# Performance work log

Measured on AMD Instinct MI355X. Metric: run time of the kernel, lower is better.

## Reference

```python
import jax, jax.numpy as jnp
import numpy as np

PIXEL_SIZE = 0.2        # Angstroms
WAVELENGTH = 0.025      # Angstroms
SLICE_THICKNESS = 2.0   # Angstroms
PH, PW = 128, 128       # probe shape


def _make_propagator(h, w, pixel, wl, dz):
    ky = jnp.fft.fftfreq(h, d=pixel).astype(jnp.float32)
    kx = jnp.fft.fftfreq(w, d=pixel).astype(jnp.float32)
    k2 = ky[:, None] ** 2 + kx[None, :] ** 2
    phase = (-jnp.pi * wl * dz) * k2
    return jnp.exp(1j * phase.astype(jnp.float32)).astype(jnp.complex64)


def setup_inputs() -> dict:
    key = jax.random.key(0)
    k0, k1, k2, k3, k4 = jax.random.split(key, 5)
    probe_real = jax.random.normal(k0, (4, PH, PW), jnp.float32)
    probe_imag = jax.random.normal(k1, (4, PH, PW), jnp.float32)
    obj_real = jax.random.normal(k2, (8, 512, 512), jnp.float32)
    obj_imag = jax.random.normal(k3, (8, 512, 512), jnp.float32)
    positions = jax.random.randint(k4, (512, 2), 0, 384).astype(jnp.int32)
    return {"probe_real": probe_real, "probe_imag": probe_imag,
            "obj_real": obj_real, "obj_imag": obj_imag,
            "positions": positions}


def reference(probe_real, probe_imag, obj_real, obj_imag, positions):
    probe = (probe_real + 1j * probe_imag).astype(jnp.complex64)  # (M,H,W)
    obj = (obj_real + 1j * obj_imag).astype(jnp.complex64)        # (S,Ho,Wo)
    num_slices = obj.shape[0]
    prop = _make_propagator(PH, PW, PIXEL_SIZE, WAVELENGTH, SLICE_THICKNESS)

    # Batched patch gather: (N, S, PH, PW)
    def get_patch(pos):
        return jax.lax.dynamic_slice(obj, (0, pos[0], pos[1]),
                                     (num_slices, PH, PW))
    patches = jax.vmap(get_patch)(positions)

    # Multislice: multiply slice 0, then [propagate, multiply] per slice.
    ex = probe[None, :, :, :] * patches[:, 0][:, None]  # (N,M,H,W)
    for s in range(1, num_slices):
        ex = jnp.fft.ifft2(jnp.fft.fft2(ex) * prop)
        ex = ex * patches[:, s][:, None]

    ex = jnp.fft.fftshift(jnp.fft.fft2(ex), axes=(-2, -1))
    intensities = jnp.sum(jnp.abs(ex) ** 2, axis=1)  # (N,H,W)
    return intensities.astype(jnp.float32)
```

## Files before the change

kernel.cpp:

```cpp
#include <hip/hip_runtime.h>
#include <hip/hip_fp16.h>
#include <math.h>

#define NT      1024
#define NPIX    16384
#define NSLICES 8
#define NMODES  4
#define OBJW    512
#define LSTR    136

typedef float v2f __attribute__((ext_vector_type(2)));

__device__ __forceinline__ v2f pk_add(v2f a, v2f b) {
    v2f d; asm("v_pk_add_f32 %0, %1, %2" : "=v"(d) : "v"(a), "v"(b)); return d;
}
__device__ __forceinline__ v2f pk_sub(v2f a, v2f b) {
    v2f d; asm("v_pk_add_f32 %0, %1, %2 neg_lo:[0,1] neg_hi:[0,1]"
               : "=v"(d) : "v"(a), "v"(b)); return d;
}
__device__ __forceinline__ v2f pk_fma(v2f a, v2f b, v2f c) {
    v2f d; asm("v_pk_fma_f32 %0, %1, %2, %3" : "=v"(d) : "v"(a), "v"(b), "v"(c)); return d;
}
__device__ __forceinline__ v2f pk_cmul(v2f a, v2f b) {
    v2f t, d;
    asm("v_pk_mul_f32 %0, %1, %2 op_sel:[0,0] op_sel_hi:[1,0]"
        : "=v"(t) : "v"(a), "v"(b));
    asm("v_pk_fma_f32 %0, %1, %2, %3 op_sel:[1,1,0] op_sel_hi:[0,1,1] neg_lo:[1,0,0]"
        : "=v"(d) : "v"(a), "v"(b), "v"(t));
    return d;
}
__device__ __forceinline__ v2f pk_cmulc(v2f a, v2f b) {
    v2f t, d;
    asm("v_pk_mul_f32 %0, %1, %2 op_sel:[0,0] op_sel_hi:[1,0]"
        : "=v"(t) : "v"(a), "v"(b));
    asm("v_pk_fma_f32 %0, %1, %2, %3 op_sel:[1,1,0] op_sel_hi:[0,1,1] neg_hi:[1,0,0]"
        : "=v"(d) : "v"(a), "v"(b), "v"(t));
    return d;
}
__device__ __forceinline__ v2f pk_mnegi(v2f a) { return (v2f){a.y, -a.x}; }
__device__ __forceinline__ v2f pk_mposi(v2f a) { return (v2f){-a.y, a.x}; }

__host__ __device__ constexpr int BR4(int p) {
    return ((p & 1) << 3) | ((p & 2) << 1) | ((p & 4) >> 1) | ((p & 8) >> 3);
}
__host__ __device__ constexpr int BR3(int c) {
    return ((c & 1) << 2) | (c & 2) | ((c & 4) >> 2);
}

__device__ __forceinline__ float xor1f(float x) {
    int i = __float_as_int(x);
    return __int_as_float(__builtin_amdgcn_update_dpp(i, i, 0xB1, 0xF, 0xF, false));
}
__device__ __forceinline__ float xor2f(float x) {
    int i = __float_as_int(x);
    return __int_as_float(__builtin_amdgcn_update_dpp(i, i, 0x4E, 0xF, 0xF, false));
}
__device__ __forceinline__ float xor4f(float x) {
    return __int_as_float(__builtin_amdgcn_ds_swizzle(__float_as_int(x), 0x101F));
}

__device__ __constant__ float FA_RE[8] = {1,1,1,1, 1.0f,  0.707106781f,  0.0f, -0.707106781f};
__device__ __constant__ float FA_IM[8] = {0,0,0,0, 0.0f, -0.707106781f, -1.0f, -0.707106781f};

__device__ __forceinline__ void fft16_fwd(v2f v[16], const v2f* W) {
    #pragma unroll
    for (int s = 8; s >= 1; s >>= 1) {
        #pragma unroll
        for (int q = 0; q < 16; q += 2 * s) {
            #pragma unroll
            for (int j = 0; j < s; j++) {
                const int tw = j * (8 / s);
                v2f u = v[q + j], w = v[q + j + s];
                v[q + j] = pk_add(u, w);
                v2f d = pk_sub(u, w);
                v[q + j + s] = (tw == 0) ? d
                             : (tw == 4) ? pk_mnegi(d)
                                         : pk_cmulc(d, W[tw]);
            }
        }
    }
}
__device__ __forceinline__ void fft16_inv(v2f v[16], const v2f* W) {
    #pragma unroll
    for (int s = 1; s <= 8; s <<= 1) {
        #pragma unroll
        for (int q = 0; q < 16; q += 2 * s) {
            #pragma unroll
            for (int j = 0; j < s; j++) {
                const int tw = j * (8 / s);
                v2f u = v[q + j], w = v[q + j + s];
                v2f tv = (tw == 0) ? w
                       : (tw == 4) ? pk_mposi(w)
                                   : pk_cmul(w, W[tw]);
                v[q + j]     = pk_add(u, tv);
                v[q + j + s] = pk_sub(u, tv);
            }
        }
    }
}

__device__ __forceinline__ void cross8_fwd(v2f v[16], v2f sAp, v2f sBp, v2f sCp,
                                           v2f fA, v2f rrf) {
    #pragma unroll
    for (int p = 0; p < 16; p++) {
        v2f o;
        o.x = xor4f(v[p].x); o.y = xor4f(v[p].y);
        v2f a = pk_fma(sAp, v[p], o);
        v2f b = pk_cmul(a, fA);
        o.x = xor2f(b.x); o.y = xor2f(b.y);
        v2f n = pk_fma(sBp, b, o);
        v2f r = pk_cmul(n, rrf);
        o.x = xor1f(r.x); o.y = xor1f(r.y);
        v[p] = pk_fma(sCp, r, o);
    }
}
__device__ __forceinline__ void cross8_inv(v2f v[16], v2f sAp, v2f sBp, v2f sCp,
                                           v2f fA, v2f rrf) {
    #pragma unroll
    for (int p = 0; p < 16; p++) {
        v2f o;
        o.x = xor1f(v[p].x); o.y = xor1f(v[p].y);
        v2f n = pk_fma(sCp, v[p], o);
        v2f r = pk_cmulc(n, rrf);
        o.x = xor2f(r.x); o.y = xor2f(r.y);
        v2f b = pk_fma(sBp, r, o);
        v2f a = pk_cmulc(b, fA);
        o.x = xor4f(a.x); o.y = xor4f(a.y);
        v[p] = pk_fma(sAp, a, o);
    }
}

__device__ __forceinline__ void pass_A_fwd(v2f v[16], int c, v2f sAp, v2f sBp,
                                           v2f sCp, v2f fA, v2f rrf,
                                           const v2f* W, const v2f* tA) {
    fft16_fwd(v, W);
    #pragma unroll
    for (int p = 0; p < 16; p++) v[p] = pk_cmul(v[p], tA[8 * p + c]);
    cross8_fwd(v, sAp, sBp, sCp, fA, rrf);
}
__device__ __forceinline__ void pass_A_inv(v2f v[16], int c, v2f sAp, v2f sBp,
                                           v2f sCp, v2f fA, v2f rrf,
                                           const v2f* W, const v2f* tA) {
    cross8_inv(v, sAp, sBp, sCp, fA, rrf);
    #pragma unroll
    for (int p = 0; p < 16; p++) v[p] = pk_cmulc(v[p], tA[8 * p + c]);
    fft16_inv(v, W);
}

__device__ __forceinline__ void pass_B_fwd(v2f v[16], int c, v2f sAp, v2f sBp,
                                           v2f sCp, v2f fA, v2f rrf,
                                           const v2f* W, const v2f* tB) {
    cross8_fwd(v, sAp, sBp, sCp, fA, rrf);
    #pragma unroll
    for (int i = 0; i < 16; i++) v[i] = pk_cmul(v[i], tB[8 * i + c]);
    fft16_fwd(v, W);
}
__device__ __forceinline__ void pass_B_inv(v2f v[16], int c, v2f sAp, v2f sBp,
                                           v2f sCp, v2f fA, v2f rrf,
                                           const v2f* W, const v2f* tB) {
    fft16_inv(v, W);
    #pragma unroll
    for (int i = 0; i < 16; i++) v[i] = pk_cmulc(v[i], tB[8 * i + c]);
    cross8_inv(v, sAp, sBp, sCp, fA, rrf);
}

__device__ __forceinline__ __half2 toh2(v2f a) {
    return __float22half2_rn(make_float2(a.x, a.y));
}
__device__ __forceinline__ v2f frh2(__half2 h) {
    float2 f = __half22float2(h);
    return (v2f){f.x, f.y};
}

__global__ void
__attribute__((amdgpu_flat_work_group_size(1024, 1024)))
multislice_kernel(const float* __restrict__ probe_re,
                  const float* __restrict__ probe_im,
                  const float* __restrict__ obj_re,
                  const float* __restrict__ obj_im,
                  const int*   __restrict__ positions,
                  float*       __restrict__ out)
{
    __shared__ __half2 LTH[128 * LSTR];
    __shared__ v2f     tA[128];
    __shared__ v2f     tB[128];
    __shared__ v2f     pytp[128];

    const int t  = threadIdx.x;
    const int g  = t >> 3;
    const int c  = t & 7;
    const int rc = BR3(c);
    const int gh = g >> 4;
    const int rho_g = ((g & 15) << 3) | gh;
    const int n  = blockIdx.x;
    const int Y0 = positions[2 * n];
    const int X0 = positions[2 * n + 1];

    if (t < 128) {
        int p_ = t >> 3, c_ = t & 7;
        float angA = -2.0f * 3.14159265358979323846f
                     * (float)(c_ * BR4(p_)) / 128.0f;
        float s, cc; __sincosf(angA, &s, &cc);
        tA[t] = (v2f){cc, s};
        float angB = -2.0f * 3.14159265358979323846f
                     * (float)(p_ * BR3(c_)) / 128.0f;
        __sincosf(angB, &s, &cc);
        tB[t] = (v2f){cc, s};
        int kh = BR3(c_) + 8 * BR4(p_);
        float fy = (float)(kh < 64 ? kh : kh - 128) * (1.0f / 25.6f);
        float ph = -0.15707963267948966f * fy * fy;
        float ps, pcs; __sincosf(ph, &ps, &pcs);
        pytp[t] = (v2f){pcs * (1.0f / 16384.0f), ps * (1.0f / 16384.0f)};
    }

    const float sA = (c < 4) ? 1.0f : -1.0f;
    const float sB = (c & 2) ? -1.0f : 1.0f;
    const float sC = (c & 1) ? -1.0f : 1.0f;
    const v2f sAp = {sA, sA}, sBp = {sB, sB}, sCp = {sC, sC};
    const v2f fA  = {FA_RE[c], FA_IM[c]};
    const v2f rrf = ((c & 3) == 3) ? (v2f){0.0f, -1.0f} : (v2f){1.0f, 0.0f};

    const v2f W[8] = {
        { 1.0f,         0.0f        },
        { 0.923879533f, 0.382683432f},
        { 0.707106781f, 0.707106781f},
        { 0.382683432f, 0.923879533f},
        { 0.0f,         1.0f        },
        {-0.382683432f, 0.923879533f},
        {-0.707106781f, 0.707106781f},
        {-0.923879533f, 0.382683432f},
    };

    float fx = (float)(g < 64 ? g : g - 128) * (1.0f / 25.6f);
    float phx = -0.15707963267948966f * fx * fx;
    float pxs, pxc; __sincosf(phx, &pxs, &pxc);
    const v2f px = {pxc, pxs};
    __syncthreads();

    const long long base = (long long)n * NPIX;
    const int a1w = rho_g ^ rc;
    const int a1r = g * LSTR + (c ^ gh);
    const int a2w = rho_g ^ c;
    const int a2r = g * LSTR + (rc ^ gh);

    v2f v[16];

    for (int m = 0; m < NMODES; m++) {
        __syncthreads();
        #pragma unroll
        for (int i = 0; i < 16; i++) {
            int w  = c + 8 * i;
            int pi = m * NPIX + g * 128 + w;
            v2f pr = {probe_re[pi], probe_im[pi]};
            int oi = (Y0 + g) * OBJW + X0 + w;
            v2f ob = {obj_re[oi], obj_im[oi]};
            v[i] = pk_cmul(pr, ob);
        }

        for (int s = 1; s < NSLICES; s++) {
            pass_A_fwd(v, c, sAp, sBp, sCp, fA, rrf, W, tA);
            #pragma unroll
            for (int p = 0; p < 16; p++) {
                int kw = BR4(p) + 16 * rc;
                LTH[kw * LSTR + a1w] = toh2(v[p]);
            }
            __syncthreads();
            #pragma unroll
            for (int i = 0; i < 16; i++)
                v[i] = frh2(LTH[a1r + 8 * i]);
            __syncthreads();
            pass_B_fwd(v, c, sAp, sBp, sCp, fA, rrf, W, tB);
            #pragma unroll
            for (int p = 0; p < 16; p++) {
                v2f pp = pk_cmul(pytp[8 * p + c], px);
                v[p] = pk_cmul(v[p], pp);
            }
            pass_B_inv(v, c, sAp, sBp, sCp, fA, rrf, W, tB);
            #pragma unroll
            for (int i = 0; i < 16; i++)
                LTH[(i + 16 * c) * LSTR + a2w] = toh2(v[i]);
            __syncthreads();
            #pragma unroll
            for (int p = 0; p < 16; p++)
                v[p] = frh2(LTH[a2r + 8 * BR4(p)]);
            __syncthreads();
            pass_A_inv(v, c, sAp, sBp, sCp, fA, rrf, W, tA);
            #pragma unroll
            for (int i = 0; i < 16; i++) {
                int w  = c + 8 * i;
                int oi = (s * OBJW + Y0 + g) * OBJW + X0 + w;
                v2f ob = {obj_re[oi], obj_im[oi]};
                v[i] = pk_cmul(v[i], ob);
            }
        }

        pass_A_fwd(v, c, sAp, sBp, sCp, fA, rrf, W, tA);
        #pragma unroll
        for (int p = 0; p < 16; p++) {
            int kw = BR4(p) + 16 * rc;
            LTH[kw * LSTR + a1w] = toh2(v[p]);
        }
        __syncthreads();
        #pragma unroll
        for (int i = 0; i < 16; i++)
            v[i] = frh2(LTH[a1r + 8 * i]);
        pass_B_fwd(v, c, sAp, sBp, sCp, fA, rrf, W, tB);
        #pragma unroll
        for (int p = 0; p < 16; p++) {
            int kh = BR3(c) + 8 * BR4(p);
            long long oidx = base + (long long)(((kh ^ 64) << 7) + (g ^ 64));
            float val = fmaf(v[p].x, v[p].x, v[p].y * v[p].y);
            if (m > 0) val += out[oidx];
            out[oidx] = val;
        }
    }
}

extern "C" void kernel_launch(void* const* d_in, const int* in_sizes, int n_in,
                              void* d_out, int out_size, void* d_ws, size_t ws_size,
                              hipStream_t stream) {
    const float* probe_re = (const float*)d_in[0];
    const float* probe_im = (const float*)d_in[1];
    const float* obj_re   = (const float*)d_in[2];
    const float* obj_im   = (const float*)d_in[3];
    const int*   pos      = (const int*)d_in[4];
    float* out = (float*)d_out;

    const int N = out_size / NPIX;
    multislice_kernel<<<dim3(N), dim3(NT), 0, stream>>>(
        probe_re, probe_im, obj_re, obj_im, pos, out);
}
```

Baseline: 1.225 ms.

## Process two probe modes per iteration with doubled LDS transpose buffers

Each thread now carries two probe modes (v and u) through the multislice FFT pipeline at once. Sharing twiddle loads, object loads and the barrier count between both modes halves the number of syncs and mode-loop iterations, and gives more independent instructions for latency hiding. The LDS transpose buffer is doubled and waves_per_eu(2) is requested to allow higher register use. The risk is register pressure and spills from holding 32 complex values per thread, plus more shared memory per block.

```diff
diff --git a/kernel.cpp b/kernel.cpp
--- a/kernel.cpp
+++ b/kernel.cpp
@@ -8,6 +8,7 @@
 #define NMODES  4
 #define OBJW    512
 #define LSTR    136
+#define BUF1    (128 * LSTR)
 
 typedef float v2f __attribute__((ext_vector_type(2)));
 
@@ -99,69 +100,106 @@
     }
 }
 
-__device__ __forceinline__ void cross8_fwd(v2f v[16], v2f sAp, v2f sBp, v2f sCp,
-                                           v2f fA, v2f rrf) {
+__device__ __forceinline__ void cross8_fwd2(v2f v[16], v2f u[16],
+                                            v2f sAp, v2f sBp, v2f sCp,
+                                            v2f fA, v2f rrf) {
     #pragma unroll
     for (int p = 0; p < 16; p++) {
-        v2f o;
+        v2f o, q;
         o.x = xor4f(v[p].x); o.y = xor4f(v[p].y);
-        v2f a = pk_fma(sAp, v[p], o);
-        v2f b = pk_cmul(a, fA);
-        o.x = xor2f(b.x); o.y = xor2f(b.y);
-        v2f n = pk_fma(sBp, b, o);
-        v2f r = pk_cmul(n, rrf);
-        o.x = xor1f(r.x); o.y = xor1f(r.y);
-        v[p] = pk_fma(sCp, r, o);
-    }
-}
-__device__ __forceinline__ void cross8_inv(v2f v[16], v2f sAp, v2f sBp, v2f sCp,
-                                           v2f fA, v2f rrf) {
+        q.x = xor4f(u[p].x); q.y = xor4f(u[p].y);
+        v2f a  = pk_fma(sAp, v[p], o);
+        v2f a2 = pk_fma(sAp, u[p], q);
+        v2f b  = pk_cmul(a,  fA);
+        v2f b2 = pk_cmul(a2, fA);
+        o.x = xor2f(b.x);  o.y = xor2f(b.y);
+        q.x = xor2f(b2.x); q.y = xor2f(b2.y);
+        v2f n  = pk_fma(sBp, b,  o);
+        v2f n2 = pk_fma(sBp, b2, q);
+        v2f r  = pk_cmul(n,  rrf);
+        v2f r2 = pk_cmul(n2, rrf);
+        o.x = xor1f(r.x);  o.y = xor1f(r.y);
+        q.x = xor1f(r2.x); q.y = xor1f(r2.y);
+        v[p] = pk_fma(sCp, r,  o);
+        u[p] = pk_fma(sCp, r2, q);
+    }
+}
+__device__ __forceinline__ void cross8_inv2(v2f v[16], v2f u[16],
+                                            v2f sAp, v2f sBp, v2f sCp,
+                                            v2f fA, v2f rrf) {
     #pragma unroll
     for (int p = 0; p < 16; p++) {
-        v2f o;
+        v2f o, q;
         o.x = xor1f(v[p].x); o.y = xor1f(v[p].y);
-        v2f n = pk_fma(sCp, v[p], o);
-        v2f r = pk_cmulc(n, rrf);
-        o.x = xor2f(r.x); o.y = xor2f(r.y);
-        v2f b = pk_fma(sBp, r, o);
-        v2f a = pk_cmulc(b, fA);
-        o.x = xor4f(a.x); o.y = xor4f(a.y);
-        v[p] = pk_fma(sAp, a, o);
-    }
-}
-
-__device__ __forceinline__ void pass_A_fwd(v2f v[16], int c, v2f sAp, v2f sBp,
-                                           v2f sCp, v2f fA, v2f rrf,
-                                           const v2f* W, const v2f* tA) {
-    fft16_fwd(v, W);
-    #pragma unroll
-    for (int p = 0; p < 16; p++) v[p] = pk_cmul(v[p], tA[8 * p + c]);
-    cross8_fwd(v, sAp, sBp, sCp, fA, rrf);
-}
-__device__ __forceinline__ void pass_A_inv(v2f v[16], int c, v2f sAp, v2f sBp,
-                                           v2f sCp, v2f fA, v2f rrf,
-                                           const v2f* W, const v2f* tA) {
-    cross8_inv(v, sAp, sBp, sCp, fA, rrf);
-    #pragma unroll
-    for (int p = 0; p < 16; p++) v[p] = pk_cmulc(v[p], tA[8 * p + c]);
-    fft16_inv(v, W);
-}
-
-__device__ __forceinline__ void pass_B_fwd(v2f v[16], int c, v2f sAp, v2f sBp,
-                                           v2f sCp, v2f fA, v2f rrf,
-                                           const v2f* W, const v2f* tB) {
-    cross8_fwd(v, sAp, sBp, sCp, fA, rrf);
-    #pragma unroll
-    for (int i = 0; i < 16; i++) v[i] = pk_cmul(v[i], tB[8 * i + c]);
-    fft16_fwd(v, W);
-}
-__device__ __forceinline__ void pass_B_inv(v2f v[16], int c, v2f sAp, v2f sBp,
-                                           v2f sCp, v2f fA, v2f rrf,
-                                           const v2f* W, const v2f* tB) {
-    fft16_inv(v, W);
-    #pragma unroll
-    for (int i = 0; i < 16; i++) v[i] = pk_cmulc(v[i], tB[8 * i + c]);
-    cross8_inv(v, sAp, sBp, sCp, fA, rrf);
+        q.x = xor1f(u[p].x); q.y = xor1f(u[p].y);
+        v2f n  = pk_fma(sCp, v[p], o);
+        v2f n2 = pk_fma(sCp, u[p], q);
+        v2f r  = pk_cmulc(n,  rrf);
+        v2f r2 = pk_cmulc(n2, rrf);
+        o.x = xor2f(r.x);  o.y = xor2f(r.y);
+        q.x = xor2f(r2.x); q.y = xor2f(r2.y);
+        v2f b  = pk_fma(sBp, r,  o);
+        v2f b2 = pk_fma(sBp, r2, q);
+        v2f a  = pk_cmulc(b,  fA);
+        v2f a2 = pk_cmulc(b2, fA);
+        o.x = xor4f(a.x);  o.y = xor4f(a.y);
+        q.x = xor4f(a2.x); q.y = xor4f(a2.y);
+        v[p] = pk_fma(sAp, a,  o);
+        u[p] = pk_fma(sAp, a2, q);
+    }
+}
+
+__device__ __forceinline__ void pass_A_fwd2(v2f v[16], v2f u[16], int c,
+                                            v2f sAp, v2f sBp, v2f sCp,
+                                            v2f fA, v2f rrf,
+                                            const v2f* W, const v2f* tA) {
+    fft16_fwd(v, W); fft16_fwd(u, W);
+    #pragma unroll
+    for (int p = 0; p < 16; p++) {
+        v2f w = tA[8 * p + c];
+        v[p] = pk_cmul(v[p], w);
+        u[p] = pk_cmul(u[p], w);
+    }
+    cross8_fwd2(v, u, sAp, sBp, sCp, fA, rrf);
+}
+__device__ __forceinline__ void pass_A_inv2(v2f v[16], v2f u[16], int c,
+                                            v2f sAp, v2f sBp, v2f sCp,
+                                            v2f fA, v2f rrf,
+                                            const v2f* W, const v2f* tA) {
+    cross8_inv2(v, u, sAp, sBp, sCp, fA, rrf);
+    #pragma unroll
+    for (int p = 0; p < 16; p++) {
+        v2f w = tA[8 * p + c];
+        v[p] = pk_cmulc(v[p], w);
+        u[p] = pk_cmulc(u[p], w);
+    }
+    fft16_inv(v, W); fft16_inv(u, W);
+}
+__device__ __forceinline__ void pass_B_fwd2(v2f v[16], v2f u[16], int c,
+                                            v2f sAp, v2f sBp, v2f sCp,
+                                            v2f fA, v2f rrf,
+                                            const v2f* W, const v2f* tB) {
+    cross8_fwd2(v, u, sAp, sBp, sCp, fA, rrf);
+    #pragma unroll
+    for (int i = 0; i < 16; i++) {
+        v2f w = tB[8 * i + c];
+        v[i] = pk_cmul(v[i], w);
+        u[i] = pk_cmul(u[i], w);
+    }
+    fft16_fwd(v, W); fft16_fwd(u, W);
+}
+__device__ __forceinline__ void pass_B_inv2(v2f v[16], v2f u[16], int c,
+                                            v2f sAp, v2f sBp, v2f sCp,
+                                            v2f fA, v2f rrf,
+                                            const v2f* W, const v2f* tB) {
+    fft16_inv(v, W); fft16_inv(u, W);
+    #pragma unroll
+    for (int i = 0; i < 16; i++) {
+        v2f w = tB[8 * i + c];
+        v[i] = pk_cmulc(v[i], w);
+        u[i] = pk_cmulc(u[i], w);
+    }
+    cross8_inv2(v, u, sAp, sBp, sCp, fA, rrf);
 }
 
 __device__ __forceinline__ __half2 toh2(v2f a) {
@@ -173,7 +211,7 @@
 }
 
 __global__ void
-__attribute__((amdgpu_flat_work_group_size(1024, 1024)))
+__attribute__((amdgpu_flat_work_group_size(1024, 1024), amdgpu_waves_per_eu(2)))
 multislice_kernel(const float* __restrict__ probe_re,
                   const float* __restrict__ probe_im,
                   const float* __restrict__ obj_re,
@@ -181,7 +219,7 @@
                   const int*   __restrict__ positions,
                   float*       __restrict__ out)
 {
-    __shared__ __half2 LTH[128 * LSTR];
+    __shared__ __half2 LTH[2 * 128 * LSTR];
     __shared__ v2f     tA[128];
     __shared__ v2f     tB[128];
     __shared__ v2f     pytp[128];
@@ -243,73 +281,89 @@
     const int a2w = rho_g ^ c;
     const int a2r = g * LSTR + (rc ^ gh);
 
-    v2f v[16];
-
-    for (int m = 0; m < NMODES; m++) {
-        __syncthreads();
+    v2f v[16], u[16];
+
+    for (int m = 0; m < NMODES; m += 2) {
         #pragma unroll
         for (int i = 0; i < 16; i++) {
             int w  = c + 8 * i;
-            int pi = m * NPIX + g * 128 + w;
-            v2f pr = {probe_re[pi], probe_im[pi]};
             int oi = (Y0 + g) * OBJW + X0 + w;
             v2f ob = {obj_re[oi], obj_im[oi]};
-            v[i] = pk_cmul(pr, ob);
+            int pi0 = m * NPIX + g * 128 + w;
+            v2f pr0 = {probe_re[pi0], probe_im[pi0]};
+            v[i] = pk_cmul(pr0, ob);
+            int pi1 = (m + 1) * NPIX + g * 128 + w;
+            v2f pr1 = {probe_re[pi1], probe_im[pi1]};
+            u[i] = pk_cmul(pr1, ob);
         }
 
         for (int s = 1; s < NSLICES; s++) {
-            pass_A_fwd(v, c, sAp, sBp, sCp, fA, rrf, W, tA);
+            pass_A_fwd2(v, u, c, sAp, sBp, sCp, fA, rrf, W, tA);
+            __syncthreads();
             #pragma unroll
             for (int p = 0; p < 16; p++) {
                 int kw = BR4(p) + 16 * rc;
-                LTH[kw * LSTR + a1w] = toh2(v[p]);
+                LTH[kw * LSTR + a1w]        = toh2(v[p]);
+                LTH[BUF1 + kw * LSTR + a1w] = toh2(u[p]);
             }
             __syncthreads();
             #pragma unroll
-            for (int i = 0; i < 16; i++)
+            for (int i = 0; i < 16; i++) {
                 v[i] = frh2(LTH[a1r + 8 * i]);
-            __syncthreads();
-            pass_B_fwd(v, c, sAp, sBp, sCp, fA, rrf, W, tB);
+                u[i] = frh2(LTH[BUF1 + a1r + 8 * i]);
+            }
+            pass_B_fwd2(v, u, c, sAp, sBp, sCp, fA, rrf, W, tB);
             #pragma unroll
             for (int p = 0; p < 16; p++) {
                 v2f pp = pk_cmul(pytp[8 * p + c], px);
                 v[p] = pk_cmul(v[p], pp);
-            }
-            pass_B_inv(v, c, sAp, sBp, sCp, fA, rrf, W, tB);
-            #pragma unroll
-            for (int i = 0; i < 16; i++)
-                LTH[(i + 16 * c) * LSTR + a2w] = toh2(v[i]);
+                u[p] = pk_cmul(u[p], pp);
+            }
+            pass_B_inv2(v, u, c, sAp, sBp, sCp, fA, rrf, W, tB);
             __syncthreads();
             #pragma unroll
-            for (int p = 0; p < 16; p++)
+            for (int i = 0; i < 16; i++) {
+                LTH[(i + 16 * c) * LSTR + a2w]        = toh2(v[i]);
+                LTH[BUF1 + (i + 16 * c) * LSTR + a2w] = toh2(u[i]);
+            }
+            __syncthreads();
+            #pragma unroll
+            for (int p = 0; p < 16; p++) {
                 v[p] = frh2(LTH[a2r + 8 * BR4(p)]);
-            __syncthreads();
-            pass_A_inv(v, c, sAp, sBp, sCp, fA, rrf, W, tA);
+                u[p] = frh2(LTH[BUF1 + a2r + 8 * BR4(p)]);
+            }
+            pass_A_inv2(v, u, c, sAp, sBp, sCp, fA, rrf, W, tA);
             #pragma unroll
             for (int i = 0; i < 16; i++) {
                 int w  = c + 8 * i;
                 int oi = (s * OBJW + Y0 + g) * OBJW + X0 + w;
                 v2f ob = {obj_re[oi], obj_im[oi]};
                 v[i] = pk_cmul(v[i], ob);
-            }
-        }
-
-        pass_A_fwd(v, c, sAp, sBp, sCp, fA, rrf, W, tA);
+                u[i] = pk_cmul(u[i], ob);
+            }
+        }
+
+        pass_A_fwd2(v, u, c, sAp, sBp, sCp, fA, rrf, W, tA);
+        __syncthreads();
         #pragma unroll
         for (int p = 0; p < 16; p++) {
             int kw = BR4(p) + 16 * rc;
-            LTH[kw * LSTR + a1w] = toh2(v[p]);
+            LTH[kw * LSTR + a1w]        = toh2(v[p]);
+            LTH[BUF1 + kw * LSTR + a1w] = toh2(u[p]);
         }
         __syncthreads();
         #pragma unroll
-        for (int i = 0; i < 16; i++)
+        for (int i = 0; i < 16; i++) {
             v[i] = frh2(LTH[a1r + 8 * i]);
-        pass_B_fwd(v, c, sAp, sBp, sCp, fA, rrf, W, tB);
+            u[i] = frh2(LTH[BUF1 + a1r + 8 * i]);
+        }
+        pass_B_fwd2(v, u, c, sAp, sBp, sCp, fA, rrf, W, tB);
         #pragma unroll
         for (int p = 0; p < 16; p++) {
             int kh = BR3(c) + 8 * BR4(p);
             long long oidx = base + (long long)(((kh ^ 64) << 7) + (g ^ 64));
             float val = fmaf(v[p].x, v[p].x, v[p].y * v[p].y);
+            val = fmaf(u[p].x, u[p].x, fmaf(u[p].y, u[p].y, val));
             if (m > 0) val += out[oidx];
             out[oidx] = val;
         }
```

Result: slower. 1.296 ms (+5.8%).
